# Kernel tuning notes

Measured on AMD Instinct MI355X. Metric: run time of the kernel, lower is better.

Reference implementation:

```python
import jax, jax.numpy as jnp
import numpy as np

V, E, H, L, B = 50000, 300, 128, 32, 8


def setup_inputs() -> dict:
    key = jax.random.key(0)
    ks = jax.random.split(key, 12)
    s = 0.05
    d = {}
    d["premise"] = jax.random.randint(ks[0], (B, L), 0, V)
    d["hypothesis"] = jax.random.randint(ks[1], (B, L), 0, V)
    d["emb"] = jax.random.normal(ks[2], (V, E), jnp.float32) * s
    d["W_ih"] = jax.random.normal(ks[3], (8 * H, 2 * E), jnp.float32) * s
    d["b_ih"] = jnp.zeros((8 * H,), jnp.float32)
    d["W_hh"] = jax.random.normal(ks[4], (8 * H, 2 * H), jnp.float32) * s
    d["b_hh"] = jnp.zeros((8 * H,), jnp.float32)
    d["W_ch"] = jax.random.normal(ks[5], (H, 2 * H), jnp.float32) * s
    d["b_ch"] = jnp.zeros((H,), jnp.float32)
    d["W_cc"] = jax.random.normal(ks[6], (H, 2 * H), jnp.float32) * s
    d["b_cc"] = jnp.zeros((H,), jnp.float32)
    d["W1"] = jax.random.normal(ks[7], (H, H), jnp.float32) * s
    d["b1"] = jnp.zeros((H,), jnp.float32)
    d["W2"] = jax.random.normal(ks[8], (H, H), jnp.float32) * s
    d["b2"] = jnp.zeros((H,), jnp.float32)
    d["W3"] = jax.random.normal(ks[9], (3, H), jnp.float32) * s
    d["b3"] = jnp.zeros((3,), jnp.float32)
    return d


def _lstm_cell(x, h, c, W_ih, b_ih, W_hh, b_hh):
    # PyTorch LSTMCell gate order: i, f, g, o
    g = x @ W_ih.T + b_ih + h @ W_hh.T + b_hh
    i, f, gg, o = jnp.split(g, 4, axis=-1)
    c_new = jax.nn.sigmoid(f) * c + jax.nn.sigmoid(i) * jnp.tanh(gg)
    h_new = jax.nn.sigmoid(o) * jnp.tanh(c_new)
    return h_new, c_new


def reference(premise, hypothesis, emb, W_ih, b_ih, W_hh, b_hh,
              W_ch, b_ch, W_cc, b_cc, W1, b1, W2, b2, W3, b3):
    p = emb[premise]      # [B, L, E]
    hyp = emb[hypothesis]  # [B, L, E]
    Bn, Ln, En = p.shape
    Hn = W_ch.shape[0]
    p_t = jnp.swapaxes(p, 0, 1)    # [L, B, E]
    hyp_t = jnp.swapaxes(hyp, 0, 1)
    z = jnp.zeros((Bn, Hn), p.dtype)

    def row_step(row_carry, p_i):
        h_up, c_up = row_carry  # [L, B, H] from previous row (left deps)

        def col_step(carry, xs):
            h_low, c_low = carry       # [B, H] from previous column (lower deps)
            h_u, c_u, x_hyp = xs       # [B,H], [B,H], [B,E]
            x = jnp.concatenate([p_i, x_hyp], axis=-1)       # [B, 2E]
            h_in = jnp.concatenate([h_u, h_low], axis=-1)    # left then lower -> [B, 2H]
            c_in = jnp.concatenate([c_u, c_low], axis=-1)
            h_o, c_o = _lstm_cell(x, h_in, c_in, W_ih, b_ih, W_hh, b_hh)
            h_n = h_o @ W_ch.T + b_ch  # condense back to [B, H]
            c_n = c_o @ W_cc.T + b_cc
            return (h_n, c_n), (h_n, c_n)

        _, (h_row, c_row) = jax.lax.scan(col_step, (z, z), (h_up, c_up, hyp_t))
        return (h_row, c_row), None

    init = (jnp.zeros((Ln, Bn, Hn), p.dtype), jnp.zeros((Ln, Bn, Hn), p.dtype))
    (h_grid, _), _ = jax.lax.scan(row_step, init, p_t)
    h = h_grid[-1]  # h[L, L] corner state, [B, H]
    h = jax.nn.relu(h @ W1.T + b1)
    h = jax.nn.relu(h @ W2.T + b2)
    return jax.nn.softmax(h @ W3.T + b3, axis=1)
```

## Files before the change

kernel.cpp:

```cpp
#include <hip/hip_runtime.h>
#include <math.h>


typedef _Float16 h2 __attribute__((ext_vector_type(2)));

__device__ __forceinline__ h2 pk_f16(float a, float b) {
    return __builtin_bit_cast(h2, __builtin_amdgcn_cvt_pkrtz(a, b));
}

#define HYP_OFF   0
#define HO_OFF    262144
#define CO_OFF    524288
#define WP_OFF    786432
#define B_OFF     1048576
#define FLAGS_OFF 1050624

#define BASE 0xAAAAAAAAu

__device__ __forceinline__ float sigm(float x) { return 1.f / (1.f + __expf(-x)); }
__device__ __forceinline__ float tanh_fast(float x) { return 1.f - 2.f / (__expf(2.f * x) + 1.f); }

__device__ __forceinline__ unsigned ld_flag(const unsigned* p) {
    return __hip_atomic_load(p, __ATOMIC_RELAXED, __HIP_MEMORY_SCOPE_AGENT);
}
__device__ __forceinline__ void st_flag(unsigned* p, unsigned v) {
    __hip_atomic_store(p, v, __ATOMIC_RELAXED, __HIP_MEMORY_SCOPE_AGENT);
}
__device__ __forceinline__ float ld_f32(const float* p) {
    unsigned u = __hip_atomic_load((const unsigned*)p, __ATOMIC_RELAXED, __HIP_MEMORY_SCOPE_AGENT);
    return __uint_as_float(u);
}
__device__ __forceinline__ void st_f32(float* p, float v) {
    __hip_atomic_store((unsigned*)p, __float_as_uint(v), __ATOMIC_RELAXED, __HIP_MEMORY_SCOPE_AGENT);
}
__device__ __forceinline__ void st_u32(unsigned* p, unsigned v) {
    __hip_atomic_store(p, v, __ATOMIC_RELAXED, __HIP_MEMORY_SCOPE_AGENT);
}
__device__ __forceinline__ float2 ld_f32x2(const float* p) {
    unsigned long long u = __hip_atomic_load((const unsigned long long*)p,
                                             __ATOMIC_RELAXED, __HIP_MEMORY_SCOPE_AGENT);
    float2 r; r.x = __uint_as_float((unsigned)u); r.y = __uint_as_float((unsigned)(u >> 32));
    return r;
}
__device__ __forceinline__ void ld_u32x2(const unsigned* p, unsigned& a, unsigned& b) {
    unsigned long long u = __hip_atomic_load((const unsigned long long*)p,
                                             __ATOMIC_RELAXED, __HIP_MEMORY_SCOPE_AGENT);
    a = (unsigned)u; b = (unsigned)(u >> 32);
}
__device__ __forceinline__ void wait_ge(const unsigned* f, unsigned target) {
    long spins = 0;
    while ((ld_flag(f) - BASE) < target) {
        __builtin_amdgcn_s_sleep(1);
        if (++spins > (1L << 22)) break;
    }
}
__device__ __forceinline__ void drain_vmem() {
    asm volatile("s_waitcnt vmcnt(0)" ::: "memory");
}

__global__ void __launch_bounds__(256, 1) grid_lstm_kernel(
    const int* __restrict__ premise, const int* __restrict__ hypothesis,
    const float* __restrict__ emb,
    const float* __restrict__ W_ih, const float* __restrict__ b_ih,
    const float* __restrict__ W_hh, const float* __restrict__ b_hh,
    const float* __restrict__ W_ch, const float* __restrict__ b_ch,
    const float* __restrict__ W_cc, const float* __restrict__ b_cc,
    const float* __restrict__ W1, const float* __restrict__ b1,
    const float* __restrict__ W2, const float* __restrict__ b2,
    const float* __restrict__ W3, const float* __restrict__ b3,
    float* __restrict__ out, float* __restrict__ ws)
{
    __shared__ h2    hAB[2048];
    __shared__ float sCo[2048];
    __shared__ float ppL[1024];
    __shared__ float red[8448];
    __shared__ float red2[2304];

    const int tid = threadIdx.x;
    const int bid = blockIdx.x;
    const int i   = bid & 31;
    const int c   = bid >> 5;

    float*    Hypproj = ws + HYP_OFF;
    float*    Ho      = ws + HO_OFF;
    float*    Co      = ws + CO_OFF;
    unsigned* WP      = (unsigned*)(ws + WP_OFF);
    float*    BU      = ws + B_OFF;
    float*    BL      = ws + B_OFF + 1024;
    unsigned* HF      = (unsigned*)(ws + FLAGS_OFF);
    unsigned* InitF   = (unsigned*)(ws + FLAGS_OFF) + 4096;

    const int tq = tid & 31, ks = tid >> 5;
    const int tl = tid & 31, bb = tid >> 5;

    {
        float* embs = red;
        for (int idx = tid; idx < 4800; idx += 256) {
            int side = idx / 2400, rem = idx - side * 2400;
            int b = rem / 300, e = rem - b * 300;
            const int* toks = side ? hypothesis : premise;
            embs[idx] = emb[(long)toks[b * 32 + i] * 300 + e];
        }
        __syncthreads();
        #pragma unroll 1
        for (int q = 0; q < 4; q++) {
            const int oo = tid + q * 256;
            const int b = oo >> 7, g = oo & 127;
            const int gr = (g >> 5) * 256 + c * 32 + (g & 31);
            float accP = b_ih[gr] + b_hh[gr];
            float accH = 0.f;
            const float* wp = W_ih + (long)gr * 600;
            const float* eP = embs + b * 300;
            const float* eH = embs + 2400 + b * 300;
            for (int e = 0; e < 300; e += 4) {
                float4 w1 = *(const float4*)(wp + e);
                float4 w2v = *(const float4*)(wp + 300 + e);
                float4 p4 = *(const float4*)(eP + e);
                float4 h4 = *(const float4*)(eH + e);
                accP += w1.x * p4.x + w1.y * p4.y + w1.z * p4.z + w1.w * p4.w;
                accH += w2v.x * h4.x + w2v.y * h4.y + w2v.z * h4.z + w2v.w * h4.w;
            }
            st_f32(&Hypproj[i * 8192 + b * 1024 + gr], accH);
            ppL[b * 128 + g] = accP;
        }
        __syncthreads();
    }

    {
        const int tr = tid >> 6, col = (tid & 63) * 4;
        const int r  = bid * 4 + tr;
        float u[4] = {0.f, 0.f, 0.f, 0.f}, l[4] = {0.f, 0.f, 0.f, 0.f};
        const float* whU = W_hh + (long)r * 256;
        const float* whL = whU + 128;
        for (int k = 0; k < 128; k++) {
            const float wu = whU[k], wl = whL[k];
            float4 wc = *(const float4*)(W_ch + (long)k * 256 + col);
            u[0] += wu * wc.x; u[1] += wu * wc.y; u[2] += wu * wc.z; u[3] += wu * wc.w;
            l[0] += wl * wc.x; l[1] += wl * wc.y; l[2] += wl * wc.z; l[3] += wl * wc.w;
        }
        unsigned* wrow = WP + (long)r * 256;
        st_u32(&wrow[col / 2],       __builtin_bit_cast(unsigned, __builtin_amdgcn_cvt_pkrtz(u[0], u[1])));
        st_u32(&wrow[col / 2 + 1],   __builtin_bit_cast(unsigned, __builtin_amdgcn_cvt_pkrtz(u[2], u[3])));
        st_u32(&wrow[128 + col / 2],     __builtin_bit_cast(unsigned, __builtin_amdgcn_cvt_pkrtz(l[0], l[1])));
        st_u32(&wrow[128 + col / 2 + 1], __builtin_bit_cast(unsigned, __builtin_amdgcn_cvt_pkrtz(l[2], l[3])));
        if ((tid & 63) == 0) {
            float su = 0.f, sl = 0.f;
            for (int k = 0; k < 128; k++) { su += whU[k] * b_ch[k]; sl += whL[k] * b_ch[k]; }
            st_f32(&BU[r], su); st_f32(&BL[r], sl);
        }
    }
    drain_vmem();
    __syncthreads();
    if (tid == 0) st_flag(&InitF[bid * 16], BASE + 1u);

    wait_ge(&InitF[tid * 16], 1u);
    __syncthreads();

    h2 w[4][32];
    #pragma unroll
    for (int a = 0; a < 4; a++) {
        const unsigned* src = WP + (long)(a * 256 + c * 32 + tq) * 256 + ks * 32;
        #pragma unroll
        for (int m = 0; m < 16; m++) {
            unsigned lo, hi;
            ld_u32x2(src + m * 2, lo, hi);
            w[a][2 * m]     = __builtin_bit_cast(h2, lo);
            w[a][2 * m + 1] = __builtin_bit_cast(h2, hi);
        }
    }
    float4 w3[8];
    {
        const float* wr = W_cc + (long)((c & 3) * 32 + tq) * 256 + ks * 32;
        #pragma unroll
        for (int m = 0; m < 8; m++) w3[m] = *(const float4*)(wr + m * 4);
    }
    float bUv[4], bLv[4];
    #pragma unroll
    for (int a = 0; a < 4; a++) {
        bUv[a] = ld_f32(&BU[a * 256 + c * 32 + tl]);
        bLv[a] = ld_f32(&BL[a * 256 + c * 32 + tl]);
    }

    #pragma unroll 1
    for (int j = 0; j < 32; j++) {
        const bool upok = (i > 0), lfok = (j > 0);
        const bool cok  = (c < 4) ? upok : lfok;
        const int  jl   = lfok ? (j - 1) : 0;

        if (upok && tid < 8)              wait_ge(&HF[((i - 1) * 8 + tid) * 16], (unsigned)(j + 1));
        if (lfok && tid >= 8 && tid < 16) wait_ge(&HF[(i * 8 + (tid - 8)) * 16], (unsigned)j);
        __syncthreads();

        float hyv[4];
        #pragma unroll
        for (int a = 0; a < 4; a++)
            hyv[a] = ld_f32(&Hypproj[j * 8192 + bb * 1024 + a * 256 + c * 32 + tl]);

        const float* HoUp = Ho + ((((i - 1) & 3) * 32 + j) * 2048);
        const float* HoLf = Ho + (((i & 3) * 32 + jl) * 2048);
        const float* CoS  = (c < 4) ? Co + ((((i - 1) & 3) * 32 + j) * 2048)
                                    : Co + (((i & 3) * 32 + jl) * 2048);
        #pragma unroll
        for (int r = 0; r < 4; r++) {
            const int idx = r * 256 + tid;
            const int b = idx >> 7, kk = idx & 127;
            float2 u = upok ? ld_f32x2(HoUp + b * 256 + 2 * kk) : make_float2(0.f, 0.f);
            float2 l = lfok ? ld_f32x2(HoLf + b * 256 + 2 * kk) : make_float2(0.f, 0.f);
            float2 cv = cok ? ld_f32x2(CoS + b * 256 + 2 * kk) : make_float2(0.f, 0.f);
            hAB[b * 256 + kk]       = pk_f16(u.x, u.y);
            hAB[b * 256 + 128 + kk] = pk_f16(l.x, l.y);
            sCo[b * 256 + 2 * kk] = cv.x; sCo[b * 256 + 2 * kk + 1] = cv.y;
        }
        __syncthreads();

        float acc[4][8], a3[8];
        #pragma unroll
        for (int a = 0; a < 4; a++)
            #pragma unroll
            for (int b = 0; b < 8; b++) acc[a][b] = 0.f;
        #pragma unroll
        for (int b = 0; b < 8; b++) a3[b] = 0.f;
        #pragma unroll
        for (int b = 0; b < 8; b++) {
            const h2*    hb = hAB + b * 256 + ks * 32;
            const float* cb = sCo + b * 256 + ks * 32;
            #pragma unroll
            for (int m4 = 0; m4 < 8; m4++) {
                uint4 hu = *(const uint4*)(hb + m4 * 4);
                h2 h0 = __builtin_bit_cast(h2, hu.x);
                h2 h1 = __builtin_bit_cast(h2, hu.y);
                h2 h2v = __builtin_bit_cast(h2, hu.z);
                h2 h3 = __builtin_bit_cast(h2, hu.w);
                #pragma unroll
                for (int a = 0; a < 4; a++) {
                    acc[a][b] = __builtin_amdgcn_fdot2(w[a][m4 * 4],     h0,  acc[a][b], false);
                    acc[a][b] = __builtin_amdgcn_fdot2(w[a][m4 * 4 + 1], h1,  acc[a][b], false);
                    acc[a][b] = __builtin_amdgcn_fdot2(w[a][m4 * 4 + 2], h2v, acc[a][b], false);
                    acc[a][b] = __builtin_amdgcn_fdot2(w[a][m4 * 4 + 3], h3,  acc[a][b], false);
                }
                float4 cv = *(const float4*)(cb + m4 * 4);
                a3[b] += w3[m4].x * cv.x + w3[m4].y * cv.y + w3[m4].z * cv.z + w3[m4].w * cv.w;
            }
        }
        #pragma unroll
        for (int a = 0; a < 4; a++)
            #pragma unroll
            for (int b = 0; b < 8; b++) red[tid * 33 + a * 8 + b] = acc[a][b];
        #pragma unroll
        for (int b = 0; b < 8; b++) red2[tid * 9 + b] = a3[b];
        __syncthreads();

        {
            float g4[4];
            #pragma unroll
            for (int a = 0; a < 4; a++) {
                float s = 0.f;
                #pragma unroll
                for (int k = 0; k < 8; k++)
                    s += red[(k * 32 + tl) * 33 + a * 8 + bb];
                s += ppL[bb * 128 + a * 32 + tl] + hyv[a];
                if (upok) s += bUv[a];
                if (lfok) s += bLv[a];
                g4[a] = s;
            }
            float ci = 0.f;
            #pragma unroll
            for (int k = 0; k < 8; k++) ci += red2[(k * 32 + tl) * 9 + bb];
            if (cok) ci += b_cc[(c & 3) * 32 + tl];
            const float cnew = sigm(g4[1]) * ci + sigm(g4[0]) * tanh_fast(g4[2]);
            const float hnew = sigm(g4[3]) * tanh_fast(cnew);
            const int base = ((i & 3) * 32 + j) * 2048 + bb * 256 + c * 32 + tl;
            st_f32(&Ho[base], hnew);
            st_f32(&Co[base], cnew);
        }
        drain_vmem();
        __syncthreads();
        if (tid == 0) st_flag(&HF[(i * 8 + c) * 16], BASE + (unsigned)(j + 1));
    }

    if (bid == 31) {
        if (tid < 8) wait_ge(&HF[(31 * 8 + tid) * 16], 32u);
        __syncthreads();
        const float* HoF = Ho + (((31 & 3) * 32 + 31) * 2048);
        #pragma unroll
        for (int r = 0; r < 4; r++) {
            const int idx = r * 256 + tid;
            float2 v = ld_f32x2(HoF + idx * 2);
            sCo[idx * 2] = v.x; sCo[idx * 2 + 1] = v.y;
        }
        __syncthreads();
        #pragma unroll 1
        for (int q = 0; q < 4; q++) {
            const int oo = tid + q * 256;
            const int b = oo >> 7, o = oo & 127;
            float a = b_ch[o];
            const float* wr = W_ch + (long)o * 256;
            const float* x = sCo + b * 256;
            for (int k = 0; k < 256; k += 4) {
                float4 wv = *(const float4*)(wr + k);
                float4 xv = *(const float4*)(x + k);
                a += wv.x * xv.x + wv.y * xv.y + wv.z * xv.z + wv.w * xv.w;
            }
            ppL[b * 128 + o] = a;
        }
        __syncthreads();
        float* m1 = red;
        float* m2 = red + 1024;
        for (int idx = tid; idx < 1024; idx += 256) {
            int b = idx >> 7, o = idx & 127;
            float a = b1[o];
            const float* wr = W1 + o * 128; const float* x = ppL + b * 128;
            for (int k = 0; k < 128; k++) a += wr[k] * x[k];
            m1[idx] = fmaxf(a, 0.f);
        }
        __syncthreads();
        for (int idx = tid; idx < 1024; idx += 256) {
            int b = idx >> 7, o = idx & 127;
            float a = b2[o];
            const float* wr = W2 + o * 128; const float* x = m1 + b * 128;
            for (int k = 0; k < 128; k++) a += wr[k] * x[k];
            m2[idx] = fmaxf(a, 0.f);
        }
        __syncthreads();
        if (tid < 8) {
            const int b = tid;
            float lg[3];
            for (int cc = 0; cc < 3; cc++) {
                float a = b3[cc];
                const float* wr = W3 + cc * 128; const float* x = m2 + b * 128;
                for (int k = 0; k < 128; k++) a += wr[k] * x[k];
                lg[cc] = a;
            }
            float m = fmaxf(lg[0], fmaxf(lg[1], lg[2]));
            float e0 = expf(lg[0] - m), e1 = expf(lg[1] - m), e2 = expf(lg[2] - m);
            float s = e0 + e1 + e2;
            out[b * 3 + 0] = e0 / s;
            out[b * 3 + 1] = e1 / s;
            out[b * 3 + 2] = e2 / s;
        }
    }
}

extern "C" void kernel_launch(void* const* d_in, const int* in_sizes, int n_in,
                              void* d_out, int out_size, void* d_ws, size_t ws_size,
                              hipStream_t stream) {
    const int*   premise    = (const int*)d_in[0];
    const int*   hypothesis = (const int*)d_in[1];
    const float* emb        = (const float*)d_in[2];
    const float* W_ih       = (const float*)d_in[3];
    const float* b_ih       = (const float*)d_in[4];
    const float* W_hh       = (const float*)d_in[5];
    const float* b_hh       = (const float*)d_in[6];
    const float* W_ch       = (const float*)d_in[7];
    const float* b_ch       = (const float*)d_in[8];
    const float* W_cc       = (const float*)d_in[9];
    const float* b_cc       = (const float*)d_in[10];
    const float* W1         = (const float*)d_in[11];
    const float* b1         = (const float*)d_in[12];
    const float* W2         = (const float*)d_in[13];
    const float* b2         = (const float*)d_in[14];
    const float* W3         = (const float*)d_in[15];
    const float* b3         = (const float*)d_in[16];
    float* out = (float*)d_out;
    float* ws  = (float*)d_ws;

    (void)in_sizes; (void)n_in; (void)out_size; (void)ws_size;

    grid_lstm_kernel<<<dim3(256), dim3(256), 0, stream>>>(
        premise, hypothesis, emb, W_ih, b_ih, W_hh, b_hh,
        W_ch, b_ch, W_cc, b_cc, W1, b1, W2, b2, W3, b3, out, ws);
}
```

Before: 816.2 us.

## Replace flag-based handoff with tagged 64-bit payloads polled directly

Each hidden/cell value is now stored as a 64-bit word whose upper half is a step tag, so consumers can poll the data itself rather than first waiting on a per-block flag and then loading. The producer-side vmem drain and barrier before the flag store are removed. Hidden states are packed to fp16 pairs before storing, which halves that traffic. A fallback path still waits on the flags and then re-sweeps. The aim is to cut inter-block handoff latency on the serial wavefront, at the cost of doubled cell-state storage and extra polling loads.

```diff
diff --git a/kernel.cpp b/kernel.cpp
--- a/kernel.cpp
+++ b/kernel.cpp
@@ -9,11 +9,13 @@
 }
 
 #define HYP_OFF   0
-#define HO_OFF    262144
-#define CO_OFF    524288
-#define WP_OFF    786432
-#define B_OFF     1048576
-#define FLAGS_OFF 1050624
+#define WP_OFF    262144
+#define B_OFF     524288
+#define INITF_OFF 526336
+#define HF_OFF    530432
+#define HOT_OFF   534528
+#define COT_OFF   796672
+#define HOF_OFF   1320960
 
 #define BASE 0xAAAAAAAAu
 
@@ -36,16 +38,11 @@
 __device__ __forceinline__ void st_u32(unsigned* p, unsigned v) {
     __hip_atomic_store(p, v, __ATOMIC_RELAXED, __HIP_MEMORY_SCOPE_AGENT);
 }
-__device__ __forceinline__ float2 ld_f32x2(const float* p) {
-    unsigned long long u = __hip_atomic_load((const unsigned long long*)p,
-                                             __ATOMIC_RELAXED, __HIP_MEMORY_SCOPE_AGENT);
-    float2 r; r.x = __uint_as_float((unsigned)u); r.y = __uint_as_float((unsigned)(u >> 32));
-    return r;
-}
-__device__ __forceinline__ void ld_u32x2(const unsigned* p, unsigned& a, unsigned& b) {
-    unsigned long long u = __hip_atomic_load((const unsigned long long*)p,
-                                             __ATOMIC_RELAXED, __HIP_MEMORY_SCOPE_AGENT);
-    a = (unsigned)u; b = (unsigned)(u >> 32);
+__device__ __forceinline__ unsigned long long ld_u64(const unsigned long long* p) {
+    return __hip_atomic_load(p, __ATOMIC_RELAXED, __HIP_MEMORY_SCOPE_AGENT);
+}
+__device__ __forceinline__ void st_u64(unsigned long long* p, unsigned long long v) {
+    __hip_atomic_store(p, v, __ATOMIC_RELAXED, __HIP_MEMORY_SCOPE_AGENT);
 }
 __device__ __forceinline__ void wait_ge(const unsigned* f, unsigned target) {
     long spins = 0;
@@ -57,6 +54,25 @@
 __device__ __forceinline__ void drain_vmem() {
     asm volatile("s_waitcnt vmcnt(0)" ::: "memory");
 }
+
+#define SWEEP_ONCE() do {                                                              \
+    _Pragma("unroll")                                                                  \
+    for (int r_ = 0; r_ < 4; r_++) {                                                   \
+        const int idx_ = r_ * 256 + tid;                                               \
+        const int b_ = idx_ >> 7, kk_ = idx_ & 127;                                    \
+        if (pend & (1u << r_))      uv[r_]  = ld_u64(HoUpT + b_ * 128 + kk_);          \
+        if (pend & (0x10u << r_))   lv[r_]  = ld_u64(HoLfT + b_ * 128 + kk_);          \
+        if (pend & (0x100u << r_))  c0v[r_] = ld_u64(CoST + b_ * 256 + 2 * kk_);       \
+        if (pend & (0x1000u << r_)) c1v[r_] = ld_u64(CoST + b_ * 256 + 2 * kk_ + 1);   \
+    }                                                                                  \
+    _Pragma("unroll")                                                                  \
+    for (int r_ = 0; r_ < 4; r_++) {                                                   \
+        if ((pend & (1u << r_))      && (unsigned)(uv[r_] >> 32)  == upTag) pend &= ~(1u << r_);      \
+        if ((pend & (0x10u << r_))   && (unsigned)(lv[r_] >> 32)  == lfTag) pend &= ~(0x10u << r_);   \
+        if ((pend & (0x100u << r_))  && (unsigned)(c0v[r_] >> 32) == coTag) pend &= ~(0x100u << r_);  \
+        if ((pend & (0x1000u << r_)) && (unsigned)(c1v[r_] >> 32) == coTag) pend &= ~(0x1000u << r_); \
+    }                                                                                  \
+} while (0)
 
 __global__ void __launch_bounds__(256, 1) grid_lstm_kernel(
     const int* __restrict__ premise, const int* __restrict__ hypothesis,
@@ -81,14 +97,15 @@
     const int i   = bid & 31;
     const int c   = bid >> 5;
 
-    float*    Hypproj = ws + HYP_OFF;
-    float*    Ho      = ws + HO_OFF;
-    float*    Co      = ws + CO_OFF;
-    unsigned* WP      = (unsigned*)(ws + WP_OFF);
-    float*    BU      = ws + B_OFF;
-    float*    BL      = ws + B_OFF + 1024;
-    unsigned* HF      = (unsigned*)(ws + FLAGS_OFF);
-    unsigned* InitF   = (unsigned*)(ws + FLAGS_OFF) + 4096;
+    float*              Hypproj = ws + HYP_OFF;
+    unsigned*           WP      = (unsigned*)(ws + WP_OFF);
+    float*              BU      = ws + B_OFF;
+    float*              BL      = ws + B_OFF + 1024;
+    unsigned*           InitF   = (unsigned*)(ws + INITF_OFF);
+    unsigned*           HF      = (unsigned*)(ws + HF_OFF);
+    unsigned long long* HoT     = (unsigned long long*)(ws + HOT_OFF);
+    unsigned long long* CoT     = (unsigned long long*)(ws + COT_OFF);
+    unsigned long long* HoF     = (unsigned long long*)(ws + HOF_OFF);
 
     const int tq = tid & 31, ks = tid >> 5;
     const int tl = tid & 31, bb = tid >> 5;
@@ -162,10 +179,9 @@
         const unsigned* src = WP + (long)(a * 256 + c * 32 + tq) * 256 + ks * 32;
         #pragma unroll
         for (int m = 0; m < 16; m++) {
-            unsigned lo, hi;
-            ld_u32x2(src + m * 2, lo, hi);
-            w[a][2 * m]     = __builtin_bit_cast(h2, lo);
-            w[a][2 * m + 1] = __builtin_bit_cast(h2, hi);
+            unsigned long long u2 = ld_u64((const unsigned long long*)(src + m * 2));
+            w[a][2 * m]     = __builtin_bit_cast(h2, (unsigned)u2);
+            w[a][2 * m + 1] = __builtin_bit_cast(h2, (unsigned)(u2 >> 32));
         }
     }
     float4 w3[8];
@@ -187,29 +203,48 @@
         const bool cok  = (c < 4) ? upok : lfok;
         const int  jl   = lfok ? (j - 1) : 0;
 
-        if (upok && tid < 8)              wait_ge(&HF[((i - 1) * 8 + tid) * 16], (unsigned)(j + 1));
-        if (lfok && tid >= 8 && tid < 16) wait_ge(&HF[(i * 8 + (tid - 8)) * 16], (unsigned)j);
-        __syncthreads();
+        const unsigned upTag = (unsigned)((i - 1) * 32 + j + 1);
+        const unsigned lfTag = (unsigned)(i * 32 + j);
+        const unsigned coTag = (c < 4) ? upTag : lfTag;
+
+        const unsigned long long* HoUpT = HoT + (size_t)(((i - 1) & 3) * 32 + j) * 1024;
+        const unsigned long long* HoLfT = HoT + (size_t)((i & 3) * 32 + jl) * 1024;
+        const unsigned long long* CoST  = (c < 4)
+            ? CoT + (size_t)(((i - 1) & 3) * 32 + j) * 2048
+            : CoT + (size_t)((i & 3) * 32 + jl) * 2048;
 
         float hyv[4];
         #pragma unroll
         for (int a = 0; a < 4; a++)
             hyv[a] = ld_f32(&Hypproj[j * 8192 + bb * 1024 + a * 256 + c * 32 + tl]);
 
-        const float* HoUp = Ho + ((((i - 1) & 3) * 32 + j) * 2048);
-        const float* HoLf = Ho + (((i & 3) * 32 + jl) * 2048);
-        const float* CoS  = (c < 4) ? Co + ((((i - 1) & 3) * 32 + j) * 2048)
-                                    : Co + (((i & 3) * 32 + jl) * 2048);
+        unsigned long long uv[4], lv[4], c0v[4], c1v[4];
+        unsigned pend = (upok ? 0x000Fu : 0u) | (lfok ? 0x00F0u : 0u) | (cok ? 0xFF00u : 0u);
+
+        SWEEP_ONCE();
+
+        if (__syncthreads_or((int)(pend != 0u))) {
+            if (upok && tid < 8)              wait_ge(&HF[((i - 1) * 8 + tid) * 16], (unsigned)(j + 1));
+            if (lfok && tid >= 8 && tid < 16) wait_ge(&HF[(i * 8 + (tid - 8)) * 16], (unsigned)j);
+            __syncthreads();
+            long spins = 0;
+            while (pend) {
+                SWEEP_ONCE();
+                if (pend) {
+                    __builtin_amdgcn_s_sleep(1);
+                    if (++spins > (1L << 20)) break;
+                }
+            }
+        }
+
         #pragma unroll
         for (int r = 0; r < 4; r++) {
             const int idx = r * 256 + tid;
             const int b = idx >> 7, kk = idx & 127;
-            float2 u = upok ? ld_f32x2(HoUp + b * 256 + 2 * kk) : make_float2(0.f, 0.f);
-            float2 l = lfok ? ld_f32x2(HoLf + b * 256 + 2 * kk) : make_float2(0.f, 0.f);
-            float2 cv = cok ? ld_f32x2(CoS + b * 256 + 2 * kk) : make_float2(0.f, 0.f);
-            hAB[b * 256 + kk]       = pk_f16(u.x, u.y);
-            hAB[b * 256 + 128 + kk] = pk_f16(l.x, l.y);
-            sCo[b * 256 + 2 * kk] = cv.x; sCo[b * 256 + 2 * kk + 1] = cv.y;
+            hAB[b * 256 + kk]       = upok ? __builtin_bit_cast(h2, (unsigned)uv[r]) : pk_f16(0.f, 0.f);
+            hAB[b * 256 + 128 + kk] = lfok ? __builtin_bit_cast(h2, (unsigned)lv[r]) : pk_f16(0.f, 0.f);
+            sCo[b * 256 + 2 * kk]     = cok ? __uint_as_float((unsigned)c0v[r]) : 0.f;
+            sCo[b * 256 + 2 * kk + 1] = cok ? __uint_as_float((unsigned)c1v[r]) : 0.f;
         }
         __syncthreads();
 
@@ -269,25 +304,49 @@
             if (cok) ci += b_cc[(c & 3) * 32 + tl];
             const float cnew = sigm(g4[1]) * ci + sigm(g4[0]) * tanh_fast(g4[2]);
             const float hnew = sigm(g4[3]) * tanh_fast(cnew);
-            const int base = ((i & 3) * 32 + j) * 2048 + bb * 256 + c * 32 + tl;
-            st_f32(&Ho[base], hnew);
-            st_f32(&Co[base], cnew);
-        }
-        drain_vmem();
-        __syncthreads();
+
+            const unsigned myTag = (unsigned)(i * 32 + j + 1);
+            const unsigned long long tagHi = ((unsigned long long)myTag) << 32;
+            const int slot = (i & 3) * 32 + j;
+
+            st_u64(&CoT[(size_t)slot * 2048 + bb * 256 + c * 32 + tl],
+                   tagHi | (unsigned long long)__float_as_uint(cnew));
+            const float hOdd = __shfl_xor(hnew, 1);
+            if ((tl & 1) == 0) {
+                const h2 pr = pk_f16(hnew, hOdd);
+                st_u64(&HoT[(size_t)slot * 1024 + bb * 128 + c * 16 + (tl >> 1)],
+                       tagHi | (unsigned long long)__builtin_bit_cast(unsigned, pr));
+            }
+            if (i == 31 && j == 31)
+                st_u64(&HoF[bb * 256 + c * 32 + tl],
+                       tagHi | (unsigned long long)__float_as_uint(hnew));
+        }
         if (tid == 0) st_flag(&HF[(i * 8 + c) * 16], BASE + (unsigned)(j + 1));
     }
 
     if (bid == 31) {
-        if (tid < 8) wait_ge(&HF[(31 * 8 + tid) * 16], 32u);
-        __syncthreads();
-        const float* HoF = Ho + (((31 & 3) * 32 + 31) * 2048);
-        #pragma unroll
-        for (int r = 0; r < 4; r++) {
-            const int idx = r * 256 + tid;
-            float2 v = ld_f32x2(HoF + idx * 2);
-            sCo[idx * 2] = v.x; sCo[idx * 2 + 1] = v.y;
-        }
+        const unsigned fTag = 1024u;
+        float hov[8] = {0.f, 0.f, 0.f, 0.f, 0.f, 0.f, 0.f, 0.f};
+        unsigned pf = 0xFFu;
+        long spins = 0;
+        while (pf) {
+            unsigned long long tv[8];
+            #pragma unroll
+            for (int r = 0; r < 8; r++)
+                if (pf & (1u << r)) tv[r] = ld_u64(HoF + r * 256 + tid);
+            #pragma unroll
+            for (int r = 0; r < 8; r++)
+                if ((pf & (1u << r)) && (unsigned)(tv[r] >> 32) == fTag) {
+                    hov[r] = __uint_as_float((unsigned)tv[r]);
+                    pf &= ~(1u << r);
+                }
+            if (pf) {
+                __builtin_amdgcn_s_sleep(1);
+                if (++spins > (1L << 22)) break;
+            }
+        }
+        #pragma unroll
+        for (int r = 0; r < 8; r++) sCo[r * 256 + tid] = hov[r];
         __syncthreads();
         #pragma unroll 1
         for (int q = 0; q < 4; q++) {
```

Result: no change. 831.7 us (+1.9%).

## Use per-wave completion flags and publish hidden state as packed fp16

Applied to the files above, without the earlier changes.

Each wave now signals its own completion flag instead of the whole block syncing before thread 0 sets one flag. Consumers wait on the 4 per-wave flags of every producer block, and a block skips waiting on its own left flags. The hidden-state exchange buffer stores packed fp16 pairs built with a lane shuffle, halving the bytes written and read per step. A separate fp32 copy of the final corner state is kept for the classifier head. This shortens the serial dependency chain between grid cells at the cost of more flag polling threads.

```diff
diff --git a/kernel.cpp b/kernel.cpp
--- a/kernel.cpp
+++ b/kernel.cpp
@@ -9,11 +9,13 @@
 }
 
 #define HYP_OFF   0
-#define HO_OFF    262144
-#define CO_OFF    524288
-#define WP_OFF    786432
-#define B_OFF     1048576
-#define FLAGS_OFF 1050624
+#define WP_OFF    262144
+#define B_OFF     524288
+#define INITF_OFF 526336
+#define WF_OFF    530432
+#define HO_OFF    546816
+#define CO_OFF    677888
+#define HOF_OFF   940032
 
 #define BASE 0xAAAAAAAAu
 
@@ -36,16 +38,13 @@
 __device__ __forceinline__ void st_u32(unsigned* p, unsigned v) {
     __hip_atomic_store(p, v, __ATOMIC_RELAXED, __HIP_MEMORY_SCOPE_AGENT);
 }
+__device__ __forceinline__ unsigned long long ld_u64(const unsigned long long* p) {
+    return __hip_atomic_load(p, __ATOMIC_RELAXED, __HIP_MEMORY_SCOPE_AGENT);
+}
 __device__ __forceinline__ float2 ld_f32x2(const float* p) {
-    unsigned long long u = __hip_atomic_load((const unsigned long long*)p,
-                                             __ATOMIC_RELAXED, __HIP_MEMORY_SCOPE_AGENT);
+    unsigned long long u = ld_u64((const unsigned long long*)p);
     float2 r; r.x = __uint_as_float((unsigned)u); r.y = __uint_as_float((unsigned)(u >> 32));
     return r;
-}
-__device__ __forceinline__ void ld_u32x2(const unsigned* p, unsigned& a, unsigned& b) {
-    unsigned long long u = __hip_atomic_load((const unsigned long long*)p,
-                                             __ATOMIC_RELAXED, __HIP_MEMORY_SCOPE_AGENT);
-    a = (unsigned)u; b = (unsigned)(u >> 32);
 }
 __device__ __forceinline__ void wait_ge(const unsigned* f, unsigned target) {
     long spins = 0;
@@ -82,13 +81,14 @@
     const int c   = bid >> 5;
 
     float*    Hypproj = ws + HYP_OFF;
-    float*    Ho      = ws + HO_OFF;
-    float*    Co      = ws + CO_OFF;
     unsigned* WP      = (unsigned*)(ws + WP_OFF);
     float*    BU      = ws + B_OFF;
     float*    BL      = ws + B_OFF + 1024;
-    unsigned* HF      = (unsigned*)(ws + FLAGS_OFF);
-    unsigned* InitF   = (unsigned*)(ws + FLAGS_OFF) + 4096;
+    unsigned* InitF   = (unsigned*)(ws + INITF_OFF);
+    unsigned* WF      = (unsigned*)(ws + WF_OFF);
+    unsigned* Ho      = (unsigned*)(ws + HO_OFF);
+    float*    Co      = ws + CO_OFF;
+    float*    HoF     = ws + HOF_OFF;
 
     const int tq = tid & 31, ks = tid >> 5;
     const int tl = tid & 31, bb = tid >> 5;
@@ -162,10 +162,9 @@
         const unsigned* src = WP + (long)(a * 256 + c * 32 + tq) * 256 + ks * 32;
         #pragma unroll
         for (int m = 0; m < 16; m++) {
-            unsigned lo, hi;
-            ld_u32x2(src + m * 2, lo, hi);
-            w[a][2 * m]     = __builtin_bit_cast(h2, lo);
-            w[a][2 * m + 1] = __builtin_bit_cast(h2, hi);
+            unsigned long long u2 = ld_u64((const unsigned long long*)(src + m * 2));
+            w[a][2 * m]     = __builtin_bit_cast(h2, (unsigned)u2);
+            w[a][2 * m + 1] = __builtin_bit_cast(h2, (unsigned)(u2 >> 32));
         }
     }
     float4 w3[8];
@@ -187,28 +186,42 @@
         const bool cok  = (c < 4) ? upok : lfok;
         const int  jl   = lfok ? (j - 1) : 0;
 
-        if (upok && tid < 8)              wait_ge(&HF[((i - 1) * 8 + tid) * 16], (unsigned)(j + 1));
-        if (lfok && tid >= 8 && tid < 16) wait_ge(&HF[(i * 8 + (tid - 8)) * 16], (unsigned)j);
-        __syncthreads();
-
         float hyv[4];
         #pragma unroll
         for (int a = 0; a < 4; a++)
             hyv[a] = ld_f32(&Hypproj[j * 8192 + bb * 1024 + a * 256 + c * 32 + tl]);
 
-        const float* HoUp = Ho + ((((i - 1) & 3) * 32 + j) * 2048);
-        const float* HoLf = Ho + (((i & 3) * 32 + jl) * 2048);
-        const float* CoS  = (c < 4) ? Co + ((((i - 1) & 3) * 32 + j) * 2048)
-                                    : Co + (((i & 3) * 32 + jl) * 2048);
+        {
+            const unsigned* fp = nullptr;
+            unsigned tgt = 0;
+            if (upok && tid < 32) {
+                fp = &WF[(((i - 1) * 8 + (tid >> 2)) * 4 + (tid & 3)) * 16];
+                tgt = (unsigned)(j + 1);
+            } else if (lfok && tid >= 32 && tid < 60) {
+                int s = tid - 32;
+                int cc = s >> 2;
+                cc += (cc >= c) ? 1 : 0;
+                fp = &WF[((i * 8 + cc) * 4 + (s & 3)) * 16];
+                tgt = (unsigned)j;
+            }
+            if (fp) wait_ge(fp, tgt);
+        }
+        __syncthreads();
+
+        const unsigned* HoUp = Ho + (size_t)(((i - 1) & 3) * 32 + j) * 1024;
+        const unsigned* HoLf = Ho + (size_t)((i & 3) * 32 + jl) * 1024;
+        const float*    CoS  = (c < 4)
+            ? Co + (size_t)(((i - 1) & 3) * 32 + j) * 2048
+            : Co + (size_t)((i & 3) * 32 + jl) * 2048;
         #pragma unroll
         for (int r = 0; r < 4; r++) {
             const int idx = r * 256 + tid;
             const int b = idx >> 7, kk = idx & 127;
-            float2 u = upok ? ld_f32x2(HoUp + b * 256 + 2 * kk) : make_float2(0.f, 0.f);
-            float2 l = lfok ? ld_f32x2(HoLf + b * 256 + 2 * kk) : make_float2(0.f, 0.f);
+            unsigned u = upok ? ld_flag(HoUp + b * 128 + kk) : 0u;
+            unsigned l = lfok ? ld_flag(HoLf + b * 128 + kk) : 0u;
             float2 cv = cok ? ld_f32x2(CoS + b * 256 + 2 * kk) : make_float2(0.f, 0.f);
-            hAB[b * 256 + kk]       = pk_f16(u.x, u.y);
-            hAB[b * 256 + 128 + kk] = pk_f16(l.x, l.y);
+            hAB[b * 256 + kk]       = __builtin_bit_cast(h2, u);
+            hAB[b * 256 + 128 + kk] = __builtin_bit_cast(h2, l);
             sCo[b * 256 + 2 * kk] = cv.x; sCo[b * 256 + 2 * kk + 1] = cv.y;
         }
         __syncthreads();
@@ -269,25 +282,28 @@
             if (cok) ci += b_cc[(c & 3) * 32 + tl];
             const float cnew = sigm(g4[1]) * ci + sigm(g4[0]) * tanh_fast(g4[2]);
             const float hnew = sigm(g4[3]) * tanh_fast(cnew);
-            const int base = ((i & 3) * 32 + j) * 2048 + bb * 256 + c * 32 + tl;
-            st_f32(&Ho[base], hnew);
-            st_f32(&Co[base], cnew);
+
+            const int slot = (i & 3) * 32 + j;
+            st_f32(&Co[(size_t)slot * 2048 + bb * 256 + c * 32 + tl], cnew);
+            const float hOdd = __shfl_xor(hnew, 1);
+            if ((tl & 1) == 0)
+                st_u32(&Ho[(size_t)slot * 1024 + bb * 128 + c * 16 + (tl >> 1)],
+                       __builtin_bit_cast(unsigned, pk_f16(hnew, hOdd)));
+            if (i == 31 && j == 31)
+                st_f32(&HoF[bb * 256 + c * 32 + tl], hnew);
         }
         drain_vmem();
-        __syncthreads();
-        if (tid == 0) st_flag(&HF[(i * 8 + c) * 16], BASE + (unsigned)(j + 1));
+        if ((tid & 63) == 0)
+            st_flag(&WF[((i * 8 + c) * 4 + (tid >> 6)) * 16], BASE + (unsigned)(j + 1));
     }
 
     if (bid == 31) {
-        if (tid < 8) wait_ge(&HF[(31 * 8 + tid) * 16], 32u);
-        __syncthreads();
-        const float* HoF = Ho + (((31 & 3) * 32 + 31) * 2048);
-        #pragma unroll
-        for (int r = 0; r < 4; r++) {
-            const int idx = r * 256 + tid;
-            float2 v = ld_f32x2(HoF + idx * 2);
-            sCo[idx * 2] = v.x; sCo[idx * 2 + 1] = v.y;
-        }
+        if (tid < 32)
+            wait_ge(&WF[((31 * 8 + (tid >> 2)) * 4 + (tid & 3)) * 16], 32u);
+        __syncthreads();
+        #pragma unroll
+        for (int r = 0; r < 8; r++)
+            sCo[r * 256 + tid] = ld_f32(&HoF[r * 256 + tid]);
         __syncthreads();
         #pragma unroll 1
         for (int q = 0; q < 4; q++) {
```

Result: faster. 795.3 us (-2.6%).
